# Optimization experiments

Hardware: AMD Instinct MI355X
Metric: run time of the kernel (lower is better)

Reference implementation:

```python
import jax, jax.numpy as jnp
import numpy as np

N, M, C = 16384, 4096, 32
R = 2.0            # max_neighbour_distance
MULT = 2.0         # neighbor_distance_multiplier
NV = 3             # voxels per axis
TV = NV * NV * NV  # 27 total grid voxels
CH = 128           # query chunk size for kNN
EPS_D = 1e-8
BN_EPS = 1e-5


def _grid_offsets():
    g = jnp.linspace(-R + R / NV, R - R / NV, NV)
    x, y, z = jnp.meshgrid(g, g, g, indexing='ij')
    return jnp.stack([x.ravel(), y.ravel(), z.ravel()], axis=-1)  # (27,3)


def _three_nn(support_xyz, new_xyz, grid_centers):
    """3-NN of each grid center among support points within a cube of half-width
    MULT*R around the parent keypoint (two-step search, neighbor_type=0 cube).
    Returns squared dists (M,27,3), idx (M,27,3), empty (M,)."""
    q = new_xyz.reshape(-1, CH, 3)
    g = grid_centers.reshape(-1, CH, TV, 3)

    def body(args):
        qc, gc = args                                   # (CH,3), (CH,27,3)
        diff = jnp.abs(support_xyz[None, :, :] - qc[:, None, :])   # (CH,N,3)
        cand = jnp.max(diff, axis=-1) <= MULT * R                   # (CH,N)
        d2 = jnp.sum((gc[:, :, None, :] - support_xyz[None, None, :, :]) ** 2,
                     axis=-1)                                       # (CH,27,N)
        d2 = jnp.where(cand[:, None, :], d2, jnp.inf)
        nd, idx = jax.lax.top_k(-d2, 3)                              # (CH,27,3)
        return -nd, idx, ~jnp.any(cand, axis=-1)

    d3, idx, empty = jax.lax.map(body, (q, g))
    d3 = jnp.where(jnp.isinf(d3), 1e10, d3)  # <3 candidates -> ~zero weight
    return (d3.reshape(-1, TV, 3), idx.reshape(-1, TV, 3), empty.reshape(-1))


def _bn_relu(x, gamma, beta):
    mu = jnp.mean(x, axis=0)
    var = jnp.var(x, axis=0)
    return jax.nn.relu((x - mu) * jax.lax.rsqrt(var + BN_EPS) * gamma + beta)


def _forward(support_xyz, support_features, new_xyz,
             w1, bn1_gamma, bn1_beta, w2, bn2_gamma, bn2_beta):
    grid_centers = new_xyz[:, None, :] + _grid_offsets()[None, :, :]  # (M,27,3)
    d3, idx, empty = _three_nn(support_xyz, new_xyz, grid_centers)
    d3 = jax.lax.stop_gradient(d3)  # torch computes kNN under no_grad

    dist_recip = 1.0 / (d3 + EPS_D)                                   # (M,27,3)
    norm = jnp.sum(dist_recip, axis=-1, keepdims=True)
    weight = dist_recip / jnp.maximum(norm, 1e-8)

    nbr_feats = support_features[idx]                 # (M,27,3,C) gather
    interp = jnp.einsum('mgk,mgkc->mgc', weight, nbr_feats)          # (M,27,C)

    nbr_xyz = support_xyz[idx]                        # (M,27,3,3)
    local_xyz = (grid_centers[:, :, None, :] - nbr_xyz).reshape(M, TV, 9)
    feats = jnp.concatenate([interp, local_xyz], axis=-1)            # (M,27,C+9)
    feats = jnp.where(empty[:, None, None], 0.0, feats)

    # grouped Conv1d (kernel 1, groups=27): per-voxel matmul
    y = jnp.einsum('mgc,goc->mgo', feats, w1).reshape(M, TV * 32)     # (M,864)
    y = _bn_relu(y, bn1_gamma, bn1_beta)
    z = y @ w2.T                                                      # (M,128)
    return _bn_relu(z, bn2_gamma, bn2_beta)


def setup_inputs() -> dict:
    key = jax.random.key(0)
    ks = jax.random.split(key, 5)
    scale = jnp.array([50.0, 50.0, 4.0])
    shift = jnp.array([0.0, 0.0, -2.0])
    support_xyz = jax.random.uniform(ks[0], (N, 3)) * scale + shift
    new_xyz = jax.random.uniform(ks[1], (M, 3)) * scale + shift
    support_features = jax.random.normal(ks[2], (N, C))
    w1 = jax.random.normal(ks[3], (TV, 32, C + 9)) * (2.0 / (C + 9)) ** 0.5
    w2 = jax.random.normal(ks[4], (128, TV * 32)) * (2.0 / (TV * 32)) ** 0.5
    return {
        'support_xyz': support_xyz,
        'support_features': support_features,
        'new_xyz': new_xyz,
        'w1': w1,
        'bn1_gamma': jnp.ones(TV * 32),
        'bn1_beta': jnp.zeros(TV * 32),
        'w2': w2,
        'bn2_gamma': jnp.ones(128),
        'bn2_beta': jnp.zeros(128),
    }


def reference(support_xyz, support_features, new_xyz,
              w1, bn1_gamma, bn1_beta, w2, bn2_gamma, bn2_beta):
    return _forward(support_xyz, support_features, new_xyz,
                    w1, bn1_gamma, bn1_beta, w2, bn2_gamma, bn2_beta)
```

## Files before the change

### kernel.cpp

```cpp
#include <hip/hip_runtime.h>
#include <hip/hip_bf16.h>

#define N_SUP 16384
#define M_Q   4096
#define TV    27
#define CIN   41
#define CH1   864
#define CH2   128
#define CAP   1024
#define NB    12

#define C2BM 16
#define C2BN 64
#define C2BK 32

__device__ __forceinline__ float gsel(int i){
  const float GOFF = (float)(-2.0 + 2.0 / 3.0);
  return (i == 0) ? GOFF : ((i == 2) ? -GOFF : 0.0f);
}

__device__ __forceinline__ int binOf(float x){
  int b = (int)(x * (float)(NB / 50.0));
  return (b < 0) ? 0 : ((b > NB - 1) ? NB - 1 : b);
}

__device__ __forceinline__ void insK(unsigned long long key,
                                     unsigned long long& k0,
                                     unsigned long long& k1,
                                     unsigned long long& k2){
  bool b0 = key < k0, b1 = key < k1, b2 = key < k2;
  k2 = b1 ? k1 : (b2 ? key : k2);
  k1 = b0 ? k0 : (b1 ? key : k1);
  k0 = b0 ? key : k0;
}

__global__ void kPre(const float* __restrict__ w1, float* __restrict__ w1T,
                     const float* __restrict__ w2, float* __restrict__ w2T,
                     const float* __restrict__ sup_xyz, int* __restrict__ counts)
{
  int idx = blockIdx.x * 256 + threadIdx.x;
  if (idx < N_SUP) {
    float x = sup_xyz[3*idx], y = sup_xyz[3*idx+1];
    atomicAdd(&counts[binOf(x) * NB + binOf(y)], 1);
  }
  if (idx < CIN * CH1) {
    int k = idx / CH1, t = idx % CH1;
    w1T[idx] = w1[(size_t)t * CIN + k];
  }
  int j = idx - CIN * CH1;
  if (j >= 0 && j < CH1 * CH2) {
    int k = j / CH2, c = j % CH2;
    w2T[j] = w2[(size_t)c * CH1 + k];
  }
}

__global__ void kScan(const int* __restrict__ counts, int* __restrict__ starts, int* __restrict__ cursor)
{
  __shared__ int sc[NB*NB];
  int t = threadIdx.x;
  if (t < NB*NB) sc[t] = counts[t];
  __syncthreads();
  if (t == 0) {
    int acc = 0;
    for (int b = 0; b < NB*NB; b++) { int c = sc[b]; sc[b] = acc; acc += c; }
  }
  __syncthreads();
  if (t < NB*NB) { starts[t] = sc[t]; cursor[t] = sc[t]; }
  if (t == NB*NB) starts[NB*NB] = N_SUP;
}

__global__ void kScatter(const float* __restrict__ sup_xyz, int* __restrict__ cursor,
                         float* __restrict__ xs, float* __restrict__ ys,
                         float* __restrict__ zs, int* __restrict__ sid)
{
  int i = blockIdx.x * 256 + threadIdx.x;
  if (i < N_SUP) {
    float x = sup_xyz[3*i], y = sup_xyz[3*i+1], z = sup_xyz[3*i+2];
    int b = binOf(x) * NB + binOf(y);
    int p = atomicAdd(&cursor[b], 1);
    xs[p] = x; ys[p] = y; zs[p] = z; sid[p] = i;
  }
}

__global__ __launch_bounds__(256) void kA12(const float* __restrict__ xs,
                                            const float* __restrict__ ys,
                                            const float* __restrict__ zs,
                                            const int*   __restrict__ sid,
                                            const int*   __restrict__ starts,
                                            const float* __restrict__ new_xyz,
                                            const float* __restrict__ sup_xyz,
                                            float* __restrict__ nnW,
                                            int*   __restrict__ nnGI,
                                            float* __restrict__ nnLX)
{
  __shared__ float4 cxyz[CAP];
  __shared__ unsigned long long sk[TV][8][3];
  __shared__ int s_cnt;

  const int m   = blockIdx.x;
  const int tid = threadIdx.x;
  if (tid == 0) s_cnt = 0;
  __syncthreads();

  const float qx = new_xyz[m*3+0];
  const float qy = new_xyz[m*3+1];
  const float qz = new_xyz[m*3+2];

  const int bx0 = binOf(qx - 4.0f), bx1 = binOf(qx + 4.0f);
  const int by0 = binOf(qy - 4.0f), by1 = binOf(qy + 4.0f);
  for (int bx = bx0; bx <= bx1; bx++) {
    const int beg = starts[bx * NB + by0];
    const int end = starts[bx * NB + by1 + 1];
    for (int i = beg + tid; i < end; i += 256) {
      float x = xs[i], y = ys[i];
      if (fabsf(__fsub_rn(x, qx)) <= 4.0f && fabsf(__fsub_rn(y, qy)) <= 4.0f) {
        int p = atomicAdd(&s_cnt, 1);
        if (p < CAP) cxyz[p] = make_float4(x, y, zs[i], __uint_as_float((unsigned)sid[i]));
      }
    }
  }
  __syncthreads();
  const int cnt = (s_cnt < CAP) ? s_cnt : CAP;

  const int v = tid >> 3, j = tid & 7;
  if (v < TV) {
    const float gx = qx + gsel(v / 9);
    const float gy = qy + gsel((v / 3) % 3);
    const float gz = qz + gsel(v % 3);
    unsigned long long k0 = ~0ull, k1 = ~0ull, k2 = ~0ull;
    float k2df = __uint_as_float(0xFFFFFFFFu);
    for (int c = j; c < cnt; c += 8) {
      float4 f4 = cxyz[c];
      float dx = __fsub_rn(gx, f4.x);
      float dy = __fsub_rn(gy, f4.y);
      float dz = __fsub_rn(gz, f4.z);
      float dd = __fadd_rn(__fadd_rn(__fmul_rn(dx,dx), __fmul_rn(dy,dy)), __fmul_rn(dz,dz));
      if (!(dd > k2df)) {
        unsigned long long key = ((unsigned long long)__float_as_uint(dd) << 32)
                               | (unsigned long long)__float_as_uint(f4.w);
        insK(key, k0, k1, k2);
        k2df = __uint_as_float((unsigned)(k2 >> 32));
      }
    }
    sk[v][j][0] = k0; sk[v][j][1] = k1; sk[v][j][2] = k2;
  }
  __syncthreads();

  if (tid < TV) {
    const int vv = tid;
    const float gx = qx + gsel(vv / 9);
    const float gy = qy + gsel((vv / 3) % 3);
    const float gz = qz + gsel(vv % 3);
    unsigned long long k0 = ~0ull, k1 = ~0ull, k2 = ~0ull;
    #pragma unroll
    for (int jj = 0; jj < 8; jj++) {
      insK(sk[vv][jj][0], k0, k1, k2);
      insK(sk[vv][jj][1], k0, k1, k2);
      insK(sk[vv][jj][2], k0, k1, k2);
    }
    const int base = m * TV + vv;
    if (cnt > 0) {
      unsigned long long ks[3] = {k0, k1, k2};
      float d[3]; int gi[3]; bool ok[3];
      #pragma unroll
      for (int r = 0; r < 3; r++) {
        unsigned db = (unsigned)(ks[r] >> 32);
        ok[r] = (db != 0xFFFFFFFFu);
        d[r]  = ok[r] ? __uint_as_float(db) : 1e10f;
        gi[r] = ok[r] ? (int)(unsigned)(ks[r] & 0xFFFFFFFFull) : 0;
      }
      float r0 = 1.0f / (d[0] + 1e-8f);
      float r1 = 1.0f / (d[1] + 1e-8f);
      float r2 = 1.0f / (d[2] + 1e-8f);
      float den = fmaxf(r0 + r1 + r2, 1e-8f);
      nnW[base*3+0] = r0 / den; nnW[base*3+1] = r1 / den; nnW[base*3+2] = r2 / den;
      nnGI[base*3+0] = gi[0]; nnGI[base*3+1] = gi[1]; nnGI[base*3+2] = gi[2];
      #pragma unroll
      for (int r = 0; r < 3; r++) {
        if (ok[r]) {
          nnLX[base*9 + r*3 + 0] = gx - sup_xyz[gi[r]*3 + 0];
          nnLX[base*9 + r*3 + 1] = gy - sup_xyz[gi[r]*3 + 1];
          nnLX[base*9 + r*3 + 2] = gz - sup_xyz[gi[r]*3 + 2];
        } else {
          nnLX[base*9 + r*3 + 0] = 0.0f;
          nnLX[base*9 + r*3 + 1] = 0.0f;
          nnLX[base*9 + r*3 + 2] = 0.0f;
        }
      }
    } else {
      #pragma unroll
      for (int r = 0; r < 3; r++) {
        nnW[base*3+r] = 0.0f; nnGI[base*3+r] = 0;
        nnLX[base*9+r*3+0] = 0.0f; nnLX[base*9+r*3+1] = 0.0f; nnLX[base*9+r*3+2] = 0.0f;
      }
    }
  }
}

__global__ __launch_bounds__(256) void kA3(const float* __restrict__ sup_feat,
                                           const float* __restrict__ nnW,
                                           const int*   __restrict__ nnGI,
                                           const float* __restrict__ nnLX,
                                           const float* __restrict__ w1T,
                                           float* __restrict__ y1,
                                           float* __restrict__ stats1)
{
  __shared__ float s_feats[8][TV][CIN];
  __shared__ float s_w[8][TV][3];
  __shared__ int   s_gi[8][TV][3];

  const int m0  = blockIdx.x * 8;
  const int tid = threadIdx.x;

  for (int t = tid; t < 8*TV*3; t += 256) {
    int q = t / (TV*3), rem = t % (TV*3);
    s_w[q][rem/3][rem%3]  = nnW[m0*TV*3 + t];
    s_gi[q][rem/3][rem%3] = nnGI[m0*TV*3 + t];
  }
  for (int t = tid; t < 8*TV*9; t += 256) {
    int q = t / (TV*9), rem = t % (TV*9);
    s_feats[q][rem/9][32 + rem%9] = nnLX[m0*TV*9 + t];
  }
  __syncthreads();

  for (int t = tid; t < 8*TV*32; t += 256) {
    const int q = t / (TV*32), rem = t % (TV*32);
    const int v = rem >> 5, ch = rem & 31;
    s_feats[q][v][ch] = s_w[q][v][0] * sup_feat[s_gi[q][v][0]*32 + ch]
                      + s_w[q][v][1] * sup_feat[s_gi[q][v][1]*32 + ch]
                      + s_w[q][v][2] * sup_feat[s_gi[q][v][2]*32 + ch];
  }
  __syncthreads();

  const int copy = (blockIdx.x & 7) * 2 * CH1;
  for (int t = tid; t < CH1; t += 256) {
    const int v = t >> 5;
    float acc[8];
    #pragma unroll
    for (int q = 0; q < 8; q++) acc[q] = 0.0f;
    for (int k = 0; k < CIN; k++) {
      float w = w1T[k * CH1 + t];
      #pragma unroll
      for (int q = 0; q < 8; q++) acc[q] += s_feats[q][v][k] * w;
    }
    float s = 0.0f, ss = 0.0f;
    #pragma unroll
    for (int q = 0; q < 8; q++) {
      y1[(size_t)(m0 + q) * CH1 + t] = acc[q];
      s += acc[q]; ss += acc[q] * acc[q];
    }
    atomicAdd(&stats1[copy + t],       s);
    atomicAdd(&stats1[copy + CH1 + t], ss);
  }
}

__global__ void kS(const float* __restrict__ stats1,
                   const float* __restrict__ g1, const float* __restrict__ b1,
                   float* __restrict__ scsg, float* __restrict__ shsg)
{
  int c = blockIdx.x * 256 + threadIdx.x;
  if (c < CH1) {
    float s = 0.0f, ssq = 0.0f;
    #pragma unroll
    for (int k = 0; k < 8; k++) {
      s   += stats1[k * 2 * CH1 + c];
      ssq += stats1[k * 2 * CH1 + CH1 + c];
    }
    float mu  = s  * (1.0f / M_Q);
    float var = ssq * (1.0f / M_Q) - mu * mu;
    float r   = 1.0f / sqrtf(var + 1e-5f);
    float gg = g1[c];
    scsg[c] = r * gg;
    shsg[c] = b1[c] - mu * r * gg;
  }
}

__global__ __launch_bounds__(256) void kC(const float* __restrict__ y1,
                                          const float* __restrict__ scsg,
                                          const float* __restrict__ shsg,
                                          const float* __restrict__ w2T,
                                          float* __restrict__ z,
                                          float* __restrict__ stats2)
{
  __shared__ float As[C2BK][21];
  __shared__ float Bs[C2BK][C2BN];
  __shared__ float st_s[2][C2BN];

  const int tid = threadIdx.x;
  const int m0  = (blockIdx.x >> 1) * C2BM;
  const int bn0 = (blockIdx.x & 1) * C2BN;

  if (tid < 2*C2BN) st_s[tid >> 6][tid & 63] = 0.0f;

  const int arow = tid >> 4;
  const int akp  = (tid & 15) * 2;
  const int bkk = tid >> 3;
  const int bc8 = (tid & 7) * 8;
  const int ty = tid >> 5;
  const int tx = tid & 31;

  float2 pa  = *(const float2*)&y1[(size_t)(m0 + arow) * CH1 + akp];
  float2 psc = *(const float2*)&scsg[akp];
  float2 psh = *(const float2*)&shsg[akp];
  float4 pb0 = *(const float4*)&w2T[(size_t)bkk * CH2 + bn0 + bc8];
  float4 pb1 = *(const float4*)&w2T[(size_t)bkk * CH2 + bn0 + bc8 + 4];

  float a00 = 0.f, a01 = 0.f, a10 = 0.f, a11 = 0.f;

  for (int k0 = 0; k0 < CH1; k0 += C2BK) {
    __syncthreads();
    As[akp  ][arow] = fmaxf(pa.x * psc.x + psh.x, 0.0f);
    As[akp+1][arow] = fmaxf(pa.y * psc.y + psh.y, 0.0f);
    *(float4*)&Bs[bkk][bc8]     = pb0;
    *(float4*)&Bs[bkk][bc8 + 4] = pb1;
    __syncthreads();
    const int kn = k0 + C2BK;
    if (kn < CH1) {
      pa  = *(const float2*)&y1[(size_t)(m0 + arow) * CH1 + kn + akp];
      psc = *(const float2*)&scsg[kn + akp];
      psh = *(const float2*)&shsg[kn + akp];
      pb0 = *(const float4*)&w2T[(size_t)(kn + bkk) * CH2 + bn0 + bc8];
      pb1 = *(const float4*)&w2T[(size_t)(kn + bkk) * CH2 + bn0 + bc8 + 4];
    }
    #pragma unroll
    for (int kk = 0; kk < C2BK; kk++) {
      float2 av = *(const float2*)&As[kk][ty*2];
      float2 bv = *(const float2*)&Bs[kk][tx*2];
      a00 += av.x*bv.x; a01 += av.x*bv.y;
      a10 += av.y*bv.x; a11 += av.y*bv.y;
    }
  }

  *(float2*)&z[(size_t)(m0 + ty*2    ) * CH2 + bn0 + tx*2] = make_float2(a00, a01);
  *(float2*)&z[(size_t)(m0 + ty*2 + 1) * CH2 + bn0 + tx*2] = make_float2(a10, a11);

  atomicAdd(&st_s[0][tx*2    ], a00 + a10);
  atomicAdd(&st_s[0][tx*2 + 1], a01 + a11);
  atomicAdd(&st_s[1][tx*2    ], a00*a00 + a10*a10);
  atomicAdd(&st_s[1][tx*2 + 1], a01*a01 + a11*a11);
  __syncthreads();
  if (tid < 2*C2BN) {
    int which = tid >> 6, c = tid & 63;
    int copy = (blockIdx.x >> 1) & 7;
    atomicAdd(&stats2[copy*256 + which*128 + bn0 + c], st_s[which][c]);
  }
}

__global__ void kD(const float* __restrict__ z,
                   const float* __restrict__ stats2,
                   const float* __restrict__ g2,
                   const float* __restrict__ b2,
                   float* __restrict__ out)
{
  int t4 = blockIdx.x * 256 + threadIdx.x;
  if (t4 >= M_Q * CH2 / 4) return;
  int c = (t4 & 31) * 4;
  float4 zv = *(const float4*)&z[(size_t)t4 * 4];
  float4 sv = make_float4(0,0,0,0), qv = make_float4(0,0,0,0);
  #pragma unroll
  for (int k = 0; k < 8; k++) {
    float4 a = *(const float4*)&stats2[k * 256 + c];
    float4 b = *(const float4*)&stats2[k * 256 + 128 + c];
    sv.x += a.x; sv.y += a.y; sv.z += a.z; sv.w += a.w;
    qv.x += b.x; qv.y += b.y; qv.z += b.z; qv.w += b.w;
  }
  float4 gv = *(const float4*)&g2[c];
  float4 bv = *(const float4*)&b2[c];
  float4 o;
  {
    float mu = sv.x * (1.0f/M_Q), var = qv.x * (1.0f/M_Q) - mu*mu;
    o.x = fmaxf((zv.x - mu) * (1.0f/sqrtf(var + 1e-5f)) * gv.x + bv.x, 0.0f);
  }
  {
    float mu = sv.y * (1.0f/M_Q), var = qv.y * (1.0f/M_Q) - mu*mu;
    o.y = fmaxf((zv.y - mu) * (1.0f/sqrtf(var + 1e-5f)) * gv.y + bv.y, 0.0f);
  }
  {
    float mu = sv.z * (1.0f/M_Q), var = qv.z * (1.0f/M_Q) - mu*mu;
    o.z = fmaxf((zv.z - mu) * (1.0f/sqrtf(var + 1e-5f)) * gv.z + bv.z, 0.0f);
  }
  {
    float mu = sv.w * (1.0f/M_Q), var = qv.w * (1.0f/M_Q) - mu*mu;
    o.w = fmaxf((zv.w - mu) * (1.0f/sqrtf(var + 1e-5f)) * gv.w + bv.w, 0.0f);
  }
  *(float4*)&out[(size_t)t4 * 4] = o;
}

extern "C" void kernel_launch(void* const* d_in, const int* in_sizes, int n_in,
                              void* d_out, int out_size, void* d_ws, size_t ws_size,
                              hipStream_t stream)
{
  const float* sup_xyz  = (const float*)d_in[0];
  const float* sup_feat = (const float*)d_in[1];
  const float* new_xyz  = (const float*)d_in[2];
  const float* w1       = (const float*)d_in[3];
  const float* g1       = (const float*)d_in[4];
  const float* b1       = (const float*)d_in[5];
  const float* w2       = (const float*)d_in[6];
  const float* g2       = (const float*)d_in[7];
  const float* b2       = (const float*)d_in[8];
  float* out = (float*)d_out;

  char* ws = (char*)d_ws;
  float* y1     = (float*)(ws);
  float* z      = (float*)(ws + 14155776);
  float* w2T    = (float*)(ws + 16252928);
  float* stats1 = (float*)(ws + 16695296);
  float* stats2 = (float*)(ws + 16750592);
  int*   counts = (int*)  (ws + 16758784);
  int*   cursor = (int*)  (ws + 16759360);
  int*   starts = (int*)  (ws + 16759936);
  float* xs     = (float*)(ws + 16760516);
  float* ys     = (float*)(ws + 16826052);
  float* zs     = (float*)(ws + 16891588);
  int*   sid    = (int*)  (ws + 16957124);
  float* nnW    = (float*)(ws + 17022660);
  int*   nnGI   = (int*)  (ws + 18349764);
  float* nnLX   = (float*)(ws + 19676868);
  float* w1T    = z;
  float* scsg   = xs;
  float* shsg   = ys;

  hipMemsetAsync(stats1, 0, 55296 + 8192 + 576 + 576, stream);

  const int PRE_TOT = CIN*CH1 + CH1*CH2;
  hipLaunchKernelGGL(kPre,    dim3((PRE_TOT + 255) / 256), dim3(256), 0, stream, w1, w1T, w2, w2T, sup_xyz, counts);
  hipLaunchKernelGGL(kScan,   dim3(1),                    dim3(256), 0, stream, counts, starts, cursor);
  hipLaunchKernelGGL(kScatter,dim3((N_SUP + 255) / 256),  dim3(256), 0, stream, sup_xyz, cursor, xs, ys, zs, sid);
  hipLaunchKernelGGL(kA12,    dim3(M_Q),                  dim3(256), 0, stream, xs, ys, zs, sid, starts, new_xyz, sup_xyz, nnW, nnGI, nnLX);
  hipLaunchKernelGGL(kA3,     dim3(M_Q / 8),              dim3(256), 0, stream, sup_feat, nnW, nnGI, nnLX, w1T, y1, stats1);
  hipLaunchKernelGGL(kS,      dim3((CH1 + 255) / 256),    dim3(256), 0, stream, stats1, g1, b1, scsg, shsg);
  hipLaunchKernelGGL(kC,      dim3((M_Q / C2BM) * 2),     dim3(256), 0, stream, y1, scsg, shsg, w2T, z, stats2);
  hipLaunchKernelGGL(kD,      dim3(M_Q * CH2 / 4 / 256),  dim3(256), 0, stream, z, stats2, g2, b2, out);
}
```

Baseline: 156.6 us.

## Use split-K with larger register tiles in second GEMM and a separate reduce kernel

The second GEMM kernel now gives each block a 32x128 output tile with a 4x4 register tile per thread, and splits K (864) into 4 chunks of 216 so there are 512 blocks. Partial results go to a workspace buffer that reuses the kNN scratch region. A new reduce kernel sums the four partials, writes z and accumulates the BN2 statistics. The aim is higher arithmetic intensity per LDS load while keeping enough blocks for parallelism. The cost is an extra launch and extra global traffic for the partial sums.

```diff
diff --git a/kernel.cpp b/kernel.cpp
--- a/kernel.cpp
+++ b/kernel.cpp
@@ -10,9 +10,9 @@
 #define CAP   1024
 #define NB    12
 
-#define C2BM 16
-#define C2BN 64
-#define C2BK 32
+#define KC_BK  24
+#define KC_KS  216
+#define KC_NCH 4
 
 __device__ __forceinline__ float gsel(int i){
   const float GOFF = (float)(-2.0 + 2.0 / 3.0);
@@ -279,71 +279,102 @@
                                           const float* __restrict__ scsg,
                                           const float* __restrict__ shsg,
                                           const float* __restrict__ w2T,
-                                          float* __restrict__ z,
-                                          float* __restrict__ stats2)
-{
-  __shared__ float As[C2BK][21];
-  __shared__ float Bs[C2BK][C2BN];
-  __shared__ float st_s[2][C2BN];
+                                          float* __restrict__ zpart)
+{
+  __shared__ float As[KC_BK][36];
+  __shared__ float Bs[KC_BK][CH2];
+  __shared__ float lsc[KC_KS], lsh[KC_KS];
 
   const int tid = threadIdx.x;
-  const int m0  = (blockIdx.x >> 1) * C2BM;
-  const int bn0 = (blockIdx.x & 1) * C2BN;
-
-  if (tid < 2*C2BN) st_s[tid >> 6][tid & 63] = 0.0f;
-
-  const int arow = tid >> 4;
-  const int akp  = (tid & 15) * 2;
-  const int bkk = tid >> 3;
-  const int bc8 = (tid & 7) * 8;
+  const int mb  = blockIdx.x & 127;
+  const int ch  = blockIdx.x >> 7;
+  const int m0  = mb * 32;
+  const int kb  = ch * KC_KS;
+
+  for (int t = tid; t < KC_KS; t += 256) { lsc[t] = scsg[kb + t]; lsh[t] = shsg[kb + t]; }
+
+  const int ar = tid >> 3;
+  const int ac = (tid & 7) * 3;
   const int ty = tid >> 5;
   const int tx = tid & 31;
 
-  float2 pa  = *(const float2*)&y1[(size_t)(m0 + arow) * CH1 + akp];
-  float2 psc = *(const float2*)&scsg[akp];
-  float2 psh = *(const float2*)&shsg[akp];
-  float4 pb0 = *(const float4*)&w2T[(size_t)bkk * CH2 + bn0 + bc8];
-  float4 pb1 = *(const float4*)&w2T[(size_t)bkk * CH2 + bn0 + bc8 + 4];
-
-  float a00 = 0.f, a01 = 0.f, a10 = 0.f, a11 = 0.f;
-
-  for (int k0 = 0; k0 < CH1; k0 += C2BK) {
+  float pa0, pa1, pa2; float4 pb[3];
+  {
+    const float* yr = &y1[(size_t)(m0 + ar) * CH1 + kb + ac];
+    pa0 = yr[0]; pa1 = yr[1]; pa2 = yr[2];
+    #pragma unroll
+    for (int jj = 0; jj < 3; jj++) {
+      int fid = tid + jj * 256; int kk = fid >> 5, c4 = (fid & 31) * 4;
+      pb[jj] = *(const float4*)&w2T[(size_t)(kb + kk) * CH2 + c4];
+    }
+  }
+
+  float acc[4][4];
+  #pragma unroll
+  for (int i = 0; i < 4; i++)
+    #pragma unroll
+    for (int jj = 0; jj < 4; jj++) acc[i][jj] = 0.0f;
+
+  for (int kt = 0; kt < KC_KS / KC_BK; kt++) {
     __syncthreads();
-    As[akp  ][arow] = fmaxf(pa.x * psc.x + psh.x, 0.0f);
-    As[akp+1][arow] = fmaxf(pa.y * psc.y + psh.y, 0.0f);
-    *(float4*)&Bs[bkk][bc8]     = pb0;
-    *(float4*)&Bs[bkk][bc8 + 4] = pb1;
+    const int kl = kt * KC_BK + ac;
+    As[ac  ][ar] = fmaxf(pa0 * lsc[kl  ] + lsh[kl  ], 0.0f);
+    As[ac+1][ar] = fmaxf(pa1 * lsc[kl+1] + lsh[kl+1], 0.0f);
+    As[ac+2][ar] = fmaxf(pa2 * lsc[kl+2] + lsh[kl+2], 0.0f);
+    #pragma unroll
+    for (int jj = 0; jj < 3; jj++) {
+      int fid = tid + jj * 256; int kk = fid >> 5, c4 = (fid & 31) * 4;
+      *(float4*)&Bs[kk][c4] = pb[jj];
+    }
     __syncthreads();
-    const int kn = k0 + C2BK;
-    if (kn < CH1) {
-      pa  = *(const float2*)&y1[(size_t)(m0 + arow) * CH1 + kn + akp];
-      psc = *(const float2*)&scsg[kn + akp];
-      psh = *(const float2*)&shsg[kn + akp];
-      pb0 = *(const float4*)&w2T[(size_t)(kn + bkk) * CH2 + bn0 + bc8];
-      pb1 = *(const float4*)&w2T[(size_t)(kn + bkk) * CH2 + bn0 + bc8 + 4];
-    }
-    #pragma unroll
-    for (int kk = 0; kk < C2BK; kk++) {
-      float2 av = *(const float2*)&As[kk][ty*2];
-      float2 bv = *(const float2*)&Bs[kk][tx*2];
-      a00 += av.x*bv.x; a01 += av.x*bv.y;
-      a10 += av.y*bv.x; a11 += av.y*bv.y;
-    }
-  }
-
-  *(float2*)&z[(size_t)(m0 + ty*2    ) * CH2 + bn0 + tx*2] = make_float2(a00, a01);
-  *(float2*)&z[(size_t)(m0 + ty*2 + 1) * CH2 + bn0 + tx*2] = make_float2(a10, a11);
-
-  atomicAdd(&st_s[0][tx*2    ], a00 + a10);
-  atomicAdd(&st_s[0][tx*2 + 1], a01 + a11);
-  atomicAdd(&st_s[1][tx*2    ], a00*a00 + a10*a10);
-  atomicAdd(&st_s[1][tx*2 + 1], a01*a01 + a11*a11);
-  __syncthreads();
-  if (tid < 2*C2BN) {
-    int which = tid >> 6, c = tid & 63;
-    int copy = (blockIdx.x >> 1) & 7;
-    atomicAdd(&stats2[copy*256 + which*128 + bn0 + c], st_s[which][c]);
-  }
+    if (kt + 1 < KC_KS / KC_BK) {
+      const float* yr = &y1[(size_t)(m0 + ar) * CH1 + kb + (kt+1) * KC_BK + ac];
+      pa0 = yr[0]; pa1 = yr[1]; pa2 = yr[2];
+      #pragma unroll
+      for (int jj = 0; jj < 3; jj++) {
+        int fid = tid + jj * 256; int kk = fid >> 5, c4 = (fid & 31) * 4;
+        pb[jj] = *(const float4*)&w2T[(size_t)(kb + (kt+1) * KC_BK + kk) * CH2 + c4];
+      }
+    }
+    #pragma unroll
+    for (int kk = 0; kk < KC_BK; kk++) {
+      float4 av = *(const float4*)&As[kk][ty*4];
+      float4 bv = *(const float4*)&Bs[kk][tx*4];
+      acc[0][0] += av.x*bv.x; acc[0][1] += av.x*bv.y; acc[0][2] += av.x*bv.z; acc[0][3] += av.x*bv.w;
+      acc[1][0] += av.y*bv.x; acc[1][1] += av.y*bv.y; acc[1][2] += av.y*bv.z; acc[1][3] += av.y*bv.w;
+      acc[2][0] += av.z*bv.x; acc[2][1] += av.z*bv.y; acc[2][2] += av.z*bv.z; acc[2][3] += av.z*bv.w;
+      acc[3][0] += av.w*bv.x; acc[3][1] += av.w*bv.y; acc[3][2] += av.w*bv.z; acc[3][3] += av.w*bv.w;
+    }
+  }
+
+  float* zp = zpart + (size_t)ch * M_Q * CH2;
+  #pragma unroll
+  for (int i = 0; i < 4; i++) {
+    *(float4*)&zp[(size_t)(m0 + ty*4 + i) * CH2 + tx*4] =
+        make_float4(acc[i][0], acc[i][1], acc[i][2], acc[i][3]);
+  }
+}
+
+__global__ void kZ(const float* __restrict__ zpart,
+                   float* __restrict__ z,
+                   float* __restrict__ stats2)
+{
+  const int tid = threadIdx.x;
+  const int c = tid & 127, h = tid >> 7;
+  const int m0 = blockIdx.x * 64 + h * 32;
+  float s = 0.0f, ss = 0.0f;
+  for (int r = 0; r < 32; r++) {
+    size_t off = (size_t)(m0 + r) * CH2 + c;
+    float v = zpart[off]
+            + zpart[off + (size_t)M_Q*CH2]
+            + zpart[off + (size_t)2*M_Q*CH2]
+            + zpart[off + (size_t)3*M_Q*CH2];
+    z[off] = v;
+    s += v; ss += v * v;
+  }
+  const int copy = (blockIdx.x & 7) * 256;
+  atomicAdd(&stats2[copy + c],       s);
+  atomicAdd(&stats2[copy + 128 + c], ss);
 }
 
 __global__ void kD(const float* __restrict__ z,
@@ -417,6 +448,7 @@
   float* nnW    = (float*)(ws + 17022660);
   int*   nnGI   = (int*)  (ws + 18349764);
   float* nnLX   = (float*)(ws + 19676868);
+  float* zpart  = (float*)(ws + 17022660);
   float* w1T    = z;
   float* scsg   = xs;
   float* shsg   = ys;
@@ -430,6 +462,7 @@
   hipLaunchKernelGGL(kA12,    dim3(M_Q),                  dim3(256), 0, stream, xs, ys, zs, sid, starts, new_xyz, sup_xyz, nnW, nnGI, nnLX);
   hipLaunchKernelGGL(kA3,     dim3(M_Q / 8),              dim3(256), 0, stream, sup_feat, nnW, nnGI, nnLX, w1T, y1, stats1);
   hipLaunchKernelGGL(kS,      dim3((CH1 + 255) / 256),    dim3(256), 0, stream, stats1, g1, b1, scsg, shsg);
-  hipLaunchKernelGGL(kC,      dim3((M_Q / C2BM) * 2),     dim3(256), 0, stream, y1, scsg, shsg, w2T, z, stats2);
+  hipLaunchKernelGGL(kC,      dim3(128 * KC_NCH),         dim3(256), 0, stream, y1, scsg, shsg, w2T, zpart);
+  hipLaunchKernelGGL(kZ,      dim3(M_Q / 64),             dim3(256), 0, stream, zpart, z, stats2);
   hipLaunchKernelGGL(kD,      dim3(M_Q * CH2 / 4 / 256),  dim3(256), 0, stream, z, stats2, g2, b2, out);
 }
```

After: 150.5 us. 3.9% less time.
